# Optimization experiments

Measured on AMD Instinct MI355X. Metric: run time of the kernel, lower is better.

## Reference

```python
import jax, jax.numpy as jnp
import numpy as np

EMBED_DIM = 64
GAMMA = 1.0
N_X = 8192
N_Y = 8192


def _self_attention(inputs, W_q, W_k):
    # inputs: [n, d]; W_q, W_k: [d, d]
    q = inputs @ W_q
    k = inputs @ W_k
    scores = jax.nn.softmax(q @ k.T / jnp.sqrt(jnp.float32(EMBED_DIM)), axis=-1)  # [n, n]
    return scores @ inputs  # [n, d]


def setup_inputs() -> dict:
    key = jax.random.key(0)
    k1, k2, k3, k4 = jax.random.split(key, 4)
    return {
        "rotation_params": jax.random.normal(k1, (EMBED_DIM, EMBED_DIM), dtype=jnp.float32),
        "entangle_params": jax.random.normal(k2, (EMBED_DIM, EMBED_DIM), dtype=jnp.float32),
        "x": jax.random.normal(k3, (N_X, EMBED_DIM), dtype=jnp.float32),
        "y": jax.random.normal(k4, (N_Y, EMBED_DIM), dtype=jnp.float32),
    }


def reference(rotation_params, entangle_params, x, y):
    x_att = _self_attention(x, rotation_params, entangle_params)  # [n_x, d]
    y_att = _self_attention(y, rotation_params, entangle_params)  # [n_y, d]
    # Pairwise squared distances, vectorizing the original per-pair loop.
    diff = x_att[:, None, :] - y_att[None, :, :]  # [n_x, n_y, d]
    sq = jnp.sum(diff * diff, axis=-1)  # [n_x, n_y]
    return jnp.exp(-GAMMA * sq)
```

## Files before the change

kernel.cpp:

```cpp
#include <hip/hip_runtime.h>
#include <math.h>

#define N 8192
#define D 64
#define LOG2E 1.4426950408889634f

typedef _Float16 half_t;
typedef _Float16 f16x8 __attribute__((ext_vector_type(8)));
typedef _Float16 f16x4 __attribute__((ext_vector_type(4)));
typedef float f32x4 __attribute__((ext_vector_type(4)));

#define MFMA32(a, b, c) __builtin_amdgcn_mfma_f32_16x16x32_f16((a), (b), (c), 0, 0, 0)

#define SPLIT(v, H, L) { half_t _h = (half_t)(v); (H) = _h; (L) = (half_t)((v) - (float)_h); }


__global__ __launch_bounds__(256) void proj_kernel(
    const float* __restrict__ Wq, const float* __restrict__ Wk,
    const float* __restrict__ X, const float* __restrict__ Y,
    float* __restrict__ Qx, float* __restrict__ Qy,
    half_t* __restrict__ Kfx, half_t* __restrict__ Kfy)
{
    __shared__ float sWq[64][64];
    __shared__ float sWk[64][64];
    __shared__ float sIn[16][64];
    const int t = threadIdx.x;
#pragma unroll
    for (int p = 0; p < 16; ++p) {
        int idx = p * 256 + t;
        sWq[idx >> 6][idx & 63] = Wq[idx];
        sWk[idx >> 6][idx & 63] = Wk[idx];
    }
    const int R0 = blockIdx.x * 16;
    const float* src; float* dq; half_t* dkf; int r0;
    if (R0 < N) { src = X; dq = Qx; dkf = Kfx; r0 = R0; }
    else        { src = Y; dq = Qy; dkf = Kfy; r0 = R0 - N; }
#pragma unroll
    for (int p = 0; p < 4; ++p) {
        int idx = p * 256 + t;
        sIn[idx >> 6][idx & 63] = src[(size_t)r0 * D + idx];
    }
    __syncthreads();
    const int c = t & 63;
    const int rb = t >> 6;
    const int ksi = c >> 5, quadi = (c >> 3) & 3, j = c & 7;
#pragma unroll
    for (int rr = 0; rr < 4; ++rr) {
        int r = rr * 4 + rb;
        float aq = 0.f, ak = 0.f;
#pragma unroll
        for (int k = 0; k < 64; ++k) {
            float xv = sIn[r][k];
            aq = fmaf(xv, sWq[k][c], aq);
            ak = fmaf(xv, sWk[k][c], ak);
        }
        int rg = r0 + r;
        dq[(size_t)rg * D + c] = aq * (0.125f * LOG2E);
        int tile = rg >> 5, tau = (rg >> 4) & 1, c16l = rg & 15;
        size_t kidx = (size_t)tile * 4096 + ksi * 2048 + tau * 1024
                    + (quadi * 16 + c16l) * 8 + j;
        half_t hh = (half_t)ak;
        dkf[kidx]       = hh;
        dkf[kidx + 512] = (half_t)(ak - (float)hh);
    }
}

__global__ __launch_bounds__(256) void ztprep_kernel(
    const float* __restrict__ X, const float* __restrict__ Y,
    half_t* __restrict__ Zfx, half_t* __restrict__ Zfy)
{
    const int t = threadIdx.x;
    const int tile = blockIdx.x;
    const float* src = blockIdx.y ? Y : X;
    half_t* dst = blockIdx.y ? Zfy : Zfx;
    const int dt = t >> 6, lane = t & 63;
    const int quad = lane >> 4, c16 = lane & 15;
    f16x8 h, l;
#pragma unroll
    for (int j = 0; j < 8; ++j) {
        float v = src[(size_t)(tile * 32 + quad * 8 + j) * D + dt * 16 + c16];
        SPLIT(v, h[j], l[j]);
    }
    half_t* d = dst + (size_t)tile * 4096 + dt * 1024 + lane * 8;
    *(f16x8*)&d[0]   = h;
    *(f16x8*)&d[512] = l;
}

template<int KS>
__global__ __launch_bounds__(256, 2) void attn_kernel(
    const float* __restrict__ Qx, const float* __restrict__ Qy,
    const half_t* __restrict__ Kfx, const half_t* __restrict__ Kfy,
    const half_t* __restrict__ Zfx, const half_t* __restrict__ Zfy,
    float* __restrict__ Opart, float* __restrict__ mpart, float* __restrict__ lpart)
{
    const int side = blockIdx.y;
    const float*  Q  = side ? Qy  : Qx;
    const half_t* Kf = side ? Kfy : Kfx;
    const half_t* Zf = side ? Zfy : Zfx;
    const int t = threadIdx.x, w = t >> 6, lane = t & 63;
    const int c16 = lane & 15, quad = lane >> 4;
    const int q0 = blockIdx.x * 128 + w * 32;
    const int tile0 = blockIdx.z * (N / KS / 32);
    const int ITERS = (N / KS) / 32;

    __shared__ half_t Pbuf[4][2][32][40];
    half_t (*Phi)[40] = Pbuf[w][0];
    half_t (*Plo)[40] = Pbuf[w][1];

    f16x8 qh[2][2], ql[2][2];
#pragma unroll
    for (int qg = 0; qg < 2; ++qg)
#pragma unroll
        for (int ks = 0; ks < 2; ++ks) {
            const float* s = &Q[(size_t)(q0 + 16 * qg + c16) * D + ks * 32 + quad * 8];
            f32x4 v0 = *(const f32x4*)s;
            f32x4 v1 = *(const f32x4*)(s + 4);
            f16x8 h, l;
#pragma unroll
            for (int i = 0; i < 4; ++i) { SPLIT(v0[i], h[i],     l[i]); }
#pragma unroll
            for (int i = 0; i < 4; ++i) { SPLIT(v1[i], h[4 + i], l[4 + i]); }
            qh[qg][ks] = h; ql[qg][ks] = l;
        }

    f32x4 ot[4][2] = {};
    f32x4 lacc[2] = {};
    float m_run[2] = {-INFINITY, -INFINITY};
    f16x8 ones;
#pragma unroll
    for (int i = 0; i < 8; ++i) ones[i] = (half_t)1.0f;

    f16x8 kAh[2][2], kAl[2][2], kBh[2][2], kBl[2][2];
    f32x4 st[2][2];

    auto loadK = [&](int tile, f16x8 (&kh)[2][2], f16x8 (&kl)[2][2]) {
        const half_t* b = Kf + (size_t)tile * 4096 + lane * 8;
#pragma unroll
        for (int ks = 0; ks < 2; ++ks)
#pragma unroll
            for (int tau = 0; tau < 2; ++tau) {
                kh[ks][tau] = *(const f16x8*)&b[ks * 2048 + tau * 1024];
                kl[ks][tau] = *(const f16x8*)&b[ks * 2048 + tau * 1024 + 512];
            }
    };
    auto doS = [&](f16x8 (&kh)[2][2], f16x8 (&kl)[2][2]) {
        const f32x4 zero = {};
#pragma unroll
        for (int qg = 0; qg < 2; ++qg)
#pragma unroll
            for (int tau = 0; tau < 2; ++tau) st[qg][tau] = zero;
#pragma unroll
        for (int ks = 0; ks < 2; ++ks)
#pragma unroll
            for (int tau = 0; tau < 2; ++tau)
#pragma unroll
                for (int qg = 0; qg < 2; ++qg) {
                    st[qg][tau] = MFMA32(kh[ks][tau], qh[qg][ks], st[qg][tau]);
                    st[qg][tau] = MFMA32(kh[ks][tau], ql[qg][ks], st[qg][tau]);
                    st[qg][tau] = MFMA32(kl[ks][tau], qh[qg][ks], st[qg][tau]);
                }
    };

    auto body = [&](int tt, f16x8 (&kh2)[2][2], f16x8 (&kl2)[2][2]) {
        const int tile = tile0 + tt;
        const half_t* zb = Zf + (size_t)tile * 4096 + lane * 8;
        f16x8 zh[4], zl[4];
#pragma unroll
        for (int dt = 0; dt < 4; ++dt) {
            zh[dt] = *(const f16x8*)&zb[dt * 1024];
            zl[dt] = *(const f16x8*)&zb[dt * 1024 + 512];
        }
        const bool more = (tt + 1 < ITERS);
        if (more) loadK(tile + 1, kh2, kl2);
#pragma unroll
        for (int qg = 0; qg < 2; ++qg) {
            float mt = fmaxf(fmaxf(fmaxf(st[qg][0][0], st[qg][0][1]),
                                   fmaxf(st[qg][0][2], st[qg][0][3])),
                             fmaxf(fmaxf(st[qg][1][0], st[qg][1][1]),
                                   fmaxf(st[qg][1][2], st[qg][1][3])));
            mt = fmaxf(mt, __shfl_xor(mt, 16));
            mt = fmaxf(mt, __shfl_xor(mt, 32));
            float mn = fmaxf(m_run[qg], mt);
            float al = exp2f(m_run[qg] - mn);
            m_run[qg] = mn;
#pragma unroll
            for (int tau = 0; tau < 2; ++tau) {
                f16x4 h4, l4;
#pragma unroll
                for (int r = 0; r < 4; ++r) {
                    float e = exp2f(st[qg][tau][r] - mn);
                    SPLIT(e, h4[r], l4[r]);
                }
                *(f16x4*)&Phi[16 * qg + c16][16 * tau + 4 * quad] = h4;
                *(f16x4*)&Plo[16 * qg + c16][16 * tau + 4 * quad] = l4;
            }
            lacc[qg] *= al;
#pragma unroll
            for (int dt = 0; dt < 4; ++dt) ot[dt][qg] *= al;
        }
        f16x8 pbh[2], pbl[2];
#pragma unroll
        for (int qg = 0; qg < 2; ++qg) {
            pbh[qg] = *(const f16x8*)&Phi[16 * qg + c16][quad * 8];
            pbl[qg] = *(const f16x8*)&Plo[16 * qg + c16][quad * 8];
        }
#pragma unroll
        for (int dt = 0; dt < 4; ++dt)
#pragma unroll
            for (int qg = 0; qg < 2; ++qg) {
                ot[dt][qg] = MFMA32(zh[dt], pbh[qg], ot[dt][qg]);
                ot[dt][qg] = MFMA32(zh[dt], pbl[qg], ot[dt][qg]);
                ot[dt][qg] = MFMA32(zl[dt], pbh[qg], ot[dt][qg]);
            }
#pragma unroll
        for (int qg = 0; qg < 2; ++qg) {
            lacc[qg] = MFMA32(ones, pbh[qg], lacc[qg]);
            lacc[qg] = MFMA32(ones, pbl[qg], lacc[qg]);
        }
        if (more) doS(kh2, kl2);
    };

    loadK(tile0, kAh, kAl);
    doS(kAh, kAl);
#pragma unroll 1
    for (int tt = 0; tt < ITERS; tt += 2) {
        body(tt,     kBh, kBl);
        body(tt + 1, kAh, kAl);
    }

    const size_t obase = (size_t)(side * KS + blockIdx.z) * N;
#pragma unroll
    for (int qg = 0; qg < 2; ++qg) {
        int q = q0 + 16 * qg + c16;
#pragma unroll
        for (int dt = 0; dt < 4; ++dt)
            *(f32x4*)&Opart[(obase + q) * D + 16 * dt + 4 * quad] = ot[dt][qg];
        if (quad == 0) {
            mpart[obase + q] = m_run[qg];
            lpart[obase + q] = lacc[qg][0];
        }
    }
}

template<int KS>
__global__ __launch_bounds__(256) void combine_kernel(
    const float* __restrict__ Opart, const float* __restrict__ mpart,
    const float* __restrict__ lpart,
    half_t* __restrict__ Xf, half_t* __restrict__ Yf,
    float* __restrict__ n2x, float* __restrict__ n2y)
{
    const int side = blockIdx.y;
    const int q = blockIdx.x * 16 + (threadIdx.x >> 4);
    const int d4 = (threadIdx.x & 15) * 4;
    float m[KS], l[KS];
#pragma unroll
    for (int s = 0; s < KS; ++s) {
        size_t b = (size_t)(side * KS + s) * N + q;
        m[s] = mpart[b]; l[s] = lpart[b];
    }
    float M = -INFINITY;
#pragma unroll
    for (int s = 0; s < KS; ++s) M = fmaxf(M, m[s]);
    float L = 0.f;
    f32x4 o = {0.f, 0.f, 0.f, 0.f};
#pragma unroll
    for (int s = 0; s < KS; ++s) {
        float sc = exp2f(m[s] - M);
        L += l[s] * sc;
        f32x4 p = *(const f32x4*)&Opart[((size_t)(side * KS + s) * N + q) * D + d4];
        o += p * sc;
    }
    float inv = 1.f / L;
    o *= inv;
    float sq = o[0] * o[0] + o[1] * o[1] + o[2] * o[2] + o[3] * o[3];
#pragma unroll
    for (int off = 1; off < 16; off <<= 1) sq += __shfl_xor(sq, off);
    half_t* dst = side ? Yf : Xf;
    float*  n2  = side ? n2y : n2x;
    if ((threadIdx.x & 15) == 0) n2[q] = sq * LOG2E;
    const float oscale = side ? 1.0f : 2.0f * LOG2E;
    f16x4 h4, l4;
#pragma unroll
    for (int i = 0; i < 4; ++i) { float v = o[i] * oscale; SPLIT(v, h4[i], l4[i]); }
    const int tile16 = q >> 4, c16l = q & 15;
    const int ksi = d4 >> 5, quadi = (d4 >> 3) & 3, j0 = d4 & 7;
    size_t idx = (size_t)tile16 * 2048 + ksi * 1024 + (quadi * 16 + c16l) * 8 + j0;
    *(f16x4*)&dst[idx]       = h4;
    *(f16x4*)&dst[idx + 512] = l4;
}

__global__ __launch_bounds__(256, 3) void rbf_kernel(
    const half_t* __restrict__ Xf, const half_t* __restrict__ Yf,
    const float* __restrict__ n2x, const float* __restrict__ n2y,
    float* __restrict__ out)
{
    const int t = threadIdx.x, w = t >> 6, lane = t & 63;
    const int c16 = lane & 15, quad = lane >> 4;
    const int X0 = blockIdx.y * 128 + (w >> 1) * 64;
    const int Y0 = blockIdx.x * 128 + (w & 1) * 64;
    float ny[4];
    f32x4 nx4[4];
#pragma unroll
    for (int yt = 0; yt < 4; ++yt) ny[yt] = n2y[Y0 + 16 * yt + c16];
#pragma unroll
    for (int xt = 0; xt < 4; ++xt)
        nx4[xt] = *(const f32x4*)&n2x[X0 + 16 * xt + 4 * quad];

    const half_t* Xb = Xf + lane * 8;
    const half_t* Yb = Yf + lane * 8;
    f32x4 acc[4][4] = {};
#pragma unroll
    for (int ks = 0; ks < 2; ++ks) {
        f16x8 bh[4], bl[4];
#pragma unroll
        for (int yt = 0; yt < 4; ++yt) {
            size_t off = (size_t)((Y0 >> 4) + yt) * 2048 + ks * 1024;
            bh[yt] = *(const f16x8*)&Yb[off];
            bl[yt] = *(const f16x8*)&Yb[off + 512];
        }
#pragma unroll
        for (int xt = 0; xt < 4; ++xt) {
            size_t ao = (size_t)((X0 >> 4) + xt) * 2048 + ks * 1024;
            f16x8 ah = *(const f16x8*)&Xb[ao];
            f16x8 al = *(const f16x8*)&Xb[ao + 512];
#pragma unroll
            for (int yt = 0; yt < 4; ++yt) {
                acc[xt][yt] = MFMA32(ah, bh[yt], acc[xt][yt]);
                acc[xt][yt] = MFMA32(ah, bl[yt], acc[xt][yt]);
                acc[xt][yt] = MFMA32(al, bh[yt], acc[xt][yt]);
            }
        }
    }
#pragma unroll
    for (int xt = 0; xt < 4; ++xt)
#pragma unroll
        for (int r = 0; r < 4; ++r) {
            int xr = X0 + 16 * xt + 4 * quad + r;
            float nx = nx4[xt][r];
#pragma unroll
            for (int yt = 0; yt < 4; ++yt) {
                float v = exp2f(acc[xt][yt][r] - nx - ny[yt]);
                out[(size_t)xr * N + Y0 + 16 * yt + c16] = v;
            }
        }
}

extern "C" void kernel_launch(void* const* d_in, const int* in_sizes, int n_in,
                              void* d_out, int out_size, void* d_ws, size_t ws_size,
                              hipStream_t stream) {
    const float* Wq = (const float*)d_in[0];
    const float* Wk = (const float*)d_in[1];
    const float* x  = (const float*)d_in[2];
    const float* y  = (const float*)d_in[3];
    float* out = (float*)d_out;

    char* p = (char*)d_ws;
    size_t used = 0;
    auto alloc = [&](size_t bytes) -> void* {
        void* r = (void*)(p + used);
        used += (bytes + 255) & ~(size_t)255;
        return r;
    };
    float*  Qx  = (float*) alloc((size_t)N * D * 4);
    float*  Qy  = (float*) alloc((size_t)N * D * 4);
    half_t* Kfx = (half_t*)alloc((size_t)N * D * 2 * 2);
    half_t* Kfy = (half_t*)alloc((size_t)N * D * 2 * 2);
    half_t* Zfx = (half_t*)alloc((size_t)N * D * 2 * 2);
    half_t* Zfy = (half_t*)alloc((size_t)N * D * 2 * 2);
    half_t* Xf  = (half_t*)alloc((size_t)N * D * 2 * 2);
    half_t* Yf  = (half_t*)alloc((size_t)N * D * 2 * 2);
    float*  n2x = (float*) alloc((size_t)N * 4);
    float*  n2y = (float*) alloc((size_t)N * 4);

    const size_t base = used;
    const size_t per_split = (size_t)2 * N * D * 4 + (size_t)2 * N * 4 * 2 + 3 * 256;
    const int KS = (ws_size >= base + 8 * per_split) ? 8 : 4;

    float* Opart = (float*)alloc((size_t)2 * KS * N * D * 4);
    float* mpart = (float*)alloc((size_t)2 * KS * N * 4);
    float* lpart = (float*)alloc((size_t)2 * KS * N * 4);

    proj_kernel<<<dim3(2 * N / 16), 256, 0, stream>>>(Wq, Wk, x, y, Qx, Qy, Kfx, Kfy);
    ztprep_kernel<<<dim3(N / 32, 2), 256, 0, stream>>>(x, y, Zfx, Zfy);
    if (KS == 8) {
        attn_kernel<8><<<dim3(N / 128, 2, 8), 256, 0, stream>>>(
            Qx, Qy, Kfx, Kfy, Zfx, Zfy, Opart, mpart, lpart);
        combine_kernel<8><<<dim3(N / 16, 2), 256, 0, stream>>>(
            Opart, mpart, lpart, Xf, Yf, n2x, n2y);
    } else {
        attn_kernel<4><<<dim3(N / 128, 2, 4), 256, 0, stream>>>(
            Qx, Qy, Kfx, Kfy, Zfx, Zfy, Opart, mpart, lpart);
        combine_kernel<4><<<dim3(N / 16, 2), 256, 0, stream>>>(
            Opart, mpart, lpart, Xf, Yf, n2x, n2y);
    }
    rbf_kernel<<<dim3(N / 128, N / 128), 256, 0, stream>>>(Xf, Yf, n2x, n2y, out);
}
```

Before: 452.9 us.

## Use single fp16 for P and Z in attention PV product; allow 16-way split

Drops the hi/lo fp16 split for the softmax probabilities and the value matrix Z, so the PV product uses one MFMA per tile instead of three and the row-sum uses one instead of two. This halves Z storage and its loads and halves the LDS P buffer. It also adds a 16-way key split when the workspace allows, for more parallelism. The cost is lower precision in the attention output, which feeds the RBF distances and exp, so accuracy may suffer, and the extra partials make the combine step heavier.

```diff
diff --git a/kernel.cpp b/kernel.cpp
--- a/kernel.cpp
+++ b/kernel.cpp
@@ -75,15 +75,11 @@
     half_t* dst = blockIdx.y ? Zfy : Zfx;
     const int dt = t >> 6, lane = t & 63;
     const int quad = lane >> 4, c16 = lane & 15;
-    f16x8 h, l;
-#pragma unroll
-    for (int j = 0; j < 8; ++j) {
-        float v = src[(size_t)(tile * 32 + quad * 8 + j) * D + dt * 16 + c16];
-        SPLIT(v, h[j], l[j]);
-    }
-    half_t* d = dst + (size_t)tile * 4096 + dt * 1024 + lane * 8;
-    *(f16x8*)&d[0]   = h;
-    *(f16x8*)&d[512] = l;
+    f16x8 h;
+#pragma unroll
+    for (int j = 0; j < 8; ++j)
+        h[j] = (half_t)src[(size_t)(tile * 32 + quad * 8 + j) * D + dt * 16 + c16];
+    *(f16x8*)&dst[(size_t)tile * 2048 + dt * 512 + lane * 8] = h;
 }
 
 template<int KS>
@@ -103,9 +99,8 @@
     const int tile0 = blockIdx.z * (N / KS / 32);
     const int ITERS = (N / KS) / 32;
 
-    __shared__ half_t Pbuf[4][2][32][40];
-    half_t (*Phi)[40] = Pbuf[w][0];
-    half_t (*Plo)[40] = Pbuf[w][1];
+    __shared__ half_t Pbuf[4][32][40];
+    half_t (*Phi)[40] = Pbuf[w];
 
     f16x8 qh[2][2], ql[2][2];
 #pragma unroll
@@ -163,13 +158,11 @@
 
     auto body = [&](int tt, f16x8 (&kh2)[2][2], f16x8 (&kl2)[2][2]) {
         const int tile = tile0 + tt;
-        const half_t* zb = Zf + (size_t)tile * 4096 + lane * 8;
-        f16x8 zh[4], zl[4];
-#pragma unroll
-        for (int dt = 0; dt < 4; ++dt) {
-            zh[dt] = *(const f16x8*)&zb[dt * 1024];
-            zl[dt] = *(const f16x8*)&zb[dt * 1024 + 512];
-        }
+        const half_t* zb = Zf + (size_t)tile * 2048 + lane * 8;
+        f16x8 zh[4];
+#pragma unroll
+        for (int dt = 0; dt < 4; ++dt)
+            zh[dt] = *(const f16x8*)&zb[dt * 512];
         const bool more = (tt + 1 < ITERS);
         if (more) loadK(tile + 1, kh2, kl2);
 #pragma unroll
@@ -185,38 +178,28 @@
             m_run[qg] = mn;
 #pragma unroll
             for (int tau = 0; tau < 2; ++tau) {
-                f16x4 h4, l4;
-#pragma unroll
-                for (int r = 0; r < 4; ++r) {
-                    float e = exp2f(st[qg][tau][r] - mn);
-                    SPLIT(e, h4[r], l4[r]);
-                }
+                f16x4 h4;
+#pragma unroll
+                for (int r = 0; r < 4; ++r)
+                    h4[r] = (half_t)exp2f(st[qg][tau][r] - mn);
                 *(f16x4*)&Phi[16 * qg + c16][16 * tau + 4 * quad] = h4;
-                *(f16x4*)&Plo[16 * qg + c16][16 * tau + 4 * quad] = l4;
             }
             lacc[qg] *= al;
 #pragma unroll
             for (int dt = 0; dt < 4; ++dt) ot[dt][qg] *= al;
         }
-        f16x8 pbh[2], pbl[2];
-#pragma unroll
-        for (int qg = 0; qg < 2; ++qg) {
+        f16x8 pbh[2];
+#pragma unroll
+        for (int qg = 0; qg < 2; ++qg)
             pbh[qg] = *(const f16x8*)&Phi[16 * qg + c16][quad * 8];
-            pbl[qg] = *(const f16x8*)&Plo[16 * qg + c16][quad * 8];
-        }
 #pragma unroll
         for (int dt = 0; dt < 4; ++dt)
 #pragma unroll
-            for (int qg = 0; qg < 2; ++qg) {
+            for (int qg = 0; qg < 2; ++qg)
                 ot[dt][qg] = MFMA32(zh[dt], pbh[qg], ot[dt][qg]);
-                ot[dt][qg] = MFMA32(zh[dt], pbl[qg], ot[dt][qg]);
-                ot[dt][qg] = MFMA32(zl[dt], pbh[qg], ot[dt][qg]);
-            }
-#pragma unroll
-        for (int qg = 0; qg < 2; ++qg) {
+#pragma unroll
+        for (int qg = 0; qg < 2; ++qg)
             lacc[qg] = MFMA32(ones, pbh[qg], lacc[qg]);
-            lacc[qg] = MFMA32(ones, pbl[qg], lacc[qg]);
-        }
         if (more) doS(kh2, kl2);
     };
 
@@ -365,8 +348,8 @@
     float*  Qy  = (float*) alloc((size_t)N * D * 4);
     half_t* Kfx = (half_t*)alloc((size_t)N * D * 2 * 2);
     half_t* Kfy = (half_t*)alloc((size_t)N * D * 2 * 2);
-    half_t* Zfx = (half_t*)alloc((size_t)N * D * 2 * 2);
-    half_t* Zfy = (half_t*)alloc((size_t)N * D * 2 * 2);
+    half_t* Zfx = (half_t*)alloc((size_t)N * D * 2);
+    half_t* Zfy = (half_t*)alloc((size_t)N * D * 2);
     half_t* Xf  = (half_t*)alloc((size_t)N * D * 2 * 2);
     half_t* Yf  = (half_t*)alloc((size_t)N * D * 2 * 2);
     float*  n2x = (float*) alloc((size_t)N * 4);
@@ -374,7 +357,9 @@
 
     const size_t base = used;
     const size_t per_split = (size_t)2 * N * D * 4 + (size_t)2 * N * 4 * 2 + 3 * 256;
-    const int KS = (ws_size >= base + 8 * per_split) ? 8 : 4;
+    int KS = 4;
+    if      (ws_size >= base + 16 * per_split) KS = 16;
+    else if (ws_size >= base +  8 * per_split) KS = 8;
 
     float* Opart = (float*)alloc((size_t)2 * KS * N * D * 4);
     float* mpart = (float*)alloc((size_t)2 * KS * N * 4);
@@ -382,7 +367,12 @@
 
     proj_kernel<<<dim3(2 * N / 16), 256, 0, stream>>>(Wq, Wk, x, y, Qx, Qy, Kfx, Kfy);
     ztprep_kernel<<<dim3(N / 32, 2), 256, 0, stream>>>(x, y, Zfx, Zfy);
-    if (KS == 8) {
+    if (KS == 16) {
+        attn_kernel<16><<<dim3(N / 128, 2, 16), 256, 0, stream>>>(
+            Qx, Qy, Kfx, Kfy, Zfx, Zfy, Opart, mpart, lpart);
+        combine_kernel<16><<<dim3(N / 16, 2), 256, 0, stream>>>(
+            Opart, mpart, lpart, Xf, Yf, n2x, n2y);
+    } else if (KS == 8) {
         attn_kernel<8><<<dim3(N / 128, 2, 8), 256, 0, stream>>>(
             Qx, Qy, Kfx, Kfy, Zfx, Zfy, Opart, mpart, lpart);
         combine_kernel<8><<<dim3(N / 16, 2), 256, 0, stream>>>(
```

Result: faster. 428.8 us (-5.3%).
